# Optimization experiments

Measured on AMD Instinct MI355X. Metric: run time of the kernel, lower is better.

## Reference

```python
import jax, jax.numpy as jnp
import numpy as np
from jax import lax

B, C, H, W = 8, 64, 256, 256
K = 10  # num_experts


def conv1x1(x, w):
    # x: [B,C,H,W], w: [O,C] (1x1 conv, no bias)
    return jnp.einsum('oc,bchw->bohw', w, x)


def dyn_conv_se(x, attn, Wk, bk, gamma):
    # Dynamic_conv2d_se with with_se=True, kernel 3, stride 1, pad 1, groups=1.
    # attn: [B,K]; Wk: [K,O,I,3,3]; bk: [K,O]; gamma: [B,O]
    aw = jnp.einsum('bk,koihw->boihw', attn, Wk)        # per-sample kernels
    ab = attn @ bk                                      # [B,O]

    def one(xi, wi):
        # xi: [C,H,W], wi: [O,I,3,3]
        return lax.conv_general_dilated(
            xi[None], wi, window_strides=(1, 1), padding='SAME',
            dimension_numbers=('NCHW', 'OIHW', 'NCHW'))[0]

    y = jax.vmap(one)(x, aw) + ab[:, :, None, None]
    return y * gamma[:, :, None, None]  # SE gain


def setup_inputs() -> dict:
    key = jax.random.key(0)
    ks = jax.random.split(key, 12)
    x = jax.random.normal(ks[0], (B, C, H, W), dtype=jnp.float32)
    logits = jax.random.uniform(ks[1], (B, K), dtype=jnp.float32)
    weights = jax.nn.softmax(logits, axis=-1)
    gamma = jax.random.uniform(ks[2], (B, C), dtype=jnp.float32)
    par = jax.random.uniform(ks[3], (B, 3, 1, H, W), dtype=jnp.float32)
    s = 0.1  # default_init_weights scale
    w1 = jax.random.normal(ks[4], (K, C, C, 3, 3), dtype=jnp.float32) * s
    b1 = jax.random.normal(ks[5], (K, C), dtype=jnp.float32) * 0.01
    w2 = jax.random.normal(ks[6], (K, C, C, 3, 3), dtype=jnp.float32) * s
    b2 = jax.random.normal(ks[7], (K, C), dtype=jnp.float32) * 0.01
    w_16x16 = jax.random.normal(ks[8], (C, C), dtype=jnp.float32) * s
    w_16x8 = jax.random.normal(ks[9], (C, C), dtype=jnp.float32) * s
    w_8x8 = jax.random.normal(ks[10], (C, C), dtype=jnp.float32) * s
    return {'x': x, 'weights': weights, 'gamma': gamma, 'par': par,
            'w1': w1, 'b1': b1, 'w2': w2, 'b2': b2,
            'w_16x16': w_16x16, 'w_16x8': w_16x8, 'w_8x8': w_8x8}


def reference(x, weights, gamma, par, w1, b1, w2, b2, w_16x16, w_16x8, w_8x8):
    # channel_first=True, sparse_val=False, one_layer=False, res_scale=1
    identity = x
    dyres = (conv1x1(x, w_16x16) * par[:, 0]
             + conv1x1(x, w_16x8) * par[:, 1]
             + conv1x1(x, w_8x8) * par[:, 2])
    out = jax.nn.relu(dyn_conv_se(x, weights, w2, b2, gamma) + dyres)
    out = dyn_conv_se(out, weights, w1, b1, gamma)
    return identity + out  # res_scale = 1
```

## Files before the change

### kernel.cpp

```cpp
#include <hip/hip_runtime.h>
#include <hip/hip_bf16.h>

typedef __attribute__((ext_vector_type(8))) short short8;
typedef __attribute__((ext_vector_type(4))) float f32x4;

#define B_ 8
#define C_ 64
#define H_ 256
#define W_ 256
#define HW_ 65536
#define K_ 10
#define NS1 24
#define NS2 18
#define HP_ 258
#define WP_ 258
#define PXP_ (HP_*WP_)
#define SLABW 34
#define SLABR 6

#define NB_COMBINE 2692
#define NB_BORDER  514
#define NB_PREP    8192

static __device__ __forceinline__ unsigned short f2bf(float f) {
    __hip_bfloat16 hb = __float2bfloat16(f);
    return *(unsigned short*)&hb;
}
static __device__ __forceinline__ float bf2f(unsigned short u) {
    unsigned v = ((unsigned)u) << 16;
    float f;
    __builtin_memcpy(&f, &v, 4);
    return f;
}

static __device__ __forceinline__ void gload_lds16(const void* g, void* l) {
    __builtin_amdgcn_global_load_lds(
        (const __attribute__((address_space(1))) unsigned int*)(unsigned long long)g,
        (__attribute__((address_space(3))) unsigned int*)(unsigned int)(unsigned long long)l,
        16, 0, 0);
}

__device__ __host__ constexpr int SDW(int ii) {
    return (ii / 6 == 0) ? 0 : ((ii / 6 == 1) ? 2 : 1);
}
__device__ __host__ constexpr int SDH(int ii) { return (ii % 6) / 2; }
__device__ __host__ constexpr int SH(int ii)  { return ii & 1; }
__device__ __host__ constexpr int SS(int ii)  {
    return ii < 18 ? (3 * SDH(ii) + SDW(ii)) * 2 + SH(ii) : ii;
}

__global__ __launch_bounds__(256) void k_pre(
    const float* __restrict__ x,
    const float* __restrict__ attn, const float* __restrict__ gamma,
    const float* __restrict__ w1, const float* __restrict__ b1,
    const float* __restrict__ w2, const float* __restrict__ b2,
    const float* __restrict__ w16, const float* __restrict__ w168,
    const float* __restrict__ w88,
    unsigned short* __restrict__ W4_1, unsigned short* __restrict__ W4_2,
    float* __restrict__ bias1, float* __restrict__ bias2,
    unsigned short* __restrict__ X1p, unsigned short* __restrict__ Tp)
{
    __shared__ float ls[64][65];
    const int bx = blockIdx.x;
    const int t = threadIdx.x;

    if (bx < NB_COMBINE) {
        const int N1 = B_ * NS1 * 2048;
        const int N2 = B_ * NS2 * 2048;
        int gid = bx * 256 + t;
        if (gid < N1) {
            int b = gid / (NS1 * 2048);
            int r = gid - b * (NS1 * 2048);
            int s = r >> 11;
            int r2 = r & 2047;
            int of = r2 >> 9, l = (r2 >> 3) & 63, j = r2 & 7;
            int o = of * 16 + (l & 15);
            int g = l >> 4;
            float val;
            if (s < 18) {
                int tp = s >> 1, h = s & 1;
                int c = h * 32 + g * 8 + j;
                float acc = 0.f;
                #pragma unroll
                for (int k = 0; k < K_; ++k)
                    acc += attn[b * K_ + k] * w2[((size_t)(k * 64 + o) * 64 + c) * 9 + tp];
                val = acc * gamma[b * 64 + o];
            } else {
                int e = s - 18;
                int m = e >> 1, h = e & 1;
                int c = h * 32 + g * 8 + j;
                const float* wm = (m == 0) ? w16 : (m == 1 ? w168 : w88);
                val = wm[o * 64 + c];
            }
            W4_1[gid] = f2bf(val);
        } else if (gid < N1 + N2) {
            int gid2 = gid - N1;
            int b = gid2 / (NS2 * 2048);
            int r = gid2 - b * (NS2 * 2048);
            int s = r >> 11;
            int r2 = r & 2047;
            int of = r2 >> 9, l = (r2 >> 3) & 63, j = r2 & 7;
            int o = of * 16 + (l & 15);
            int g = l >> 4;
            int tp = s >> 1, h = s & 1;
            int c = h * 32 + g * 8 + j;
            float acc = 0.f;
            #pragma unroll
            for (int k = 0; k < K_; ++k)
                acc += attn[b * K_ + k] * w1[((size_t)(k * 64 + o) * 64 + c) * 9 + tp];
            W4_2[gid2] = f2bf(acc * gamma[b * 64 + o]);
        } else if (gid < N1 + N2 + 1024) {
            int id2 = gid - N1 - N2;
            int b = id2 >> 7;
            int rest = id2 & 127;
            int o = rest >> 1;
            int which = rest & 1;
            const float* bb = which ? b1 : b2;
            float acc = 0.f;
            #pragma unroll
            for (int k = 0; k < K_; ++k) acc += attn[b * K_ + k] * bb[k * 64 + o];
            float v = acc * gamma[b * 64 + o];
            if (which) bias2[b * 64 + o] = v; else bias1[b * 64 + o] = v;
        }
    } else if (bx < NB_COMBINE + NB_BORDER) {
        int gid = (bx - NB_COMBINE) * 256 + t;
        if (gid >= 2 * B_ * 1028 * 8) return;
        int chunk = gid & 7;
        int rest = gid >> 3;
        int p = rest % 1028;
        int rb = rest / 1028;
        int buf = rb & 1, b = rb >> 1;
        int row, col;
        if (p < 258) { row = 0; col = p; }
        else if (p < 516) { row = 257; col = p - 258; }
        else if (p < 772) { row = p - 516 + 1; col = 0; }
        else { row = p - 772 + 1; col = 257; }
        unsigned short* base = (buf ? Tp : X1p) +
            ((size_t)b * PXP_ + (size_t)row * WP_ + col) * 64 + chunk * 8;
        *(short8*)base = (short8){0, 0, 0, 0, 0, 0, 0, 0};
    } else {
        int pb = bx - (NB_COMBINE + NB_BORDER);
        const int b = pb >> 10;
        const int px0 = (pb & 1023) * 64;
        const int row = px0 >> 8;
        const int col0 = px0 & 255;
        #pragma unroll
        for (int it = 0; it < 4; ++it) {
            int e = t + it * 256;
            int ch = e >> 4, q = e & 15;
            f32x4 v = *(const f32x4*)(x + ((size_t)(b * 64 + ch)) * HW_ + px0 + q * 4);
            ls[ch][q * 4 + 0] = v[0];
            ls[ch][q * 4 + 1] = v[1];
            ls[ch][q * 4 + 2] = v[2];
            ls[ch][q * 4 + 3] = v[3];
        }
        __syncthreads();
        unsigned short* dst = X1p + ((size_t)b * PXP_ + (size_t)(row + 1) * WP_ + col0 + 1) * 64;
        #pragma unroll
        for (int k = 0; k < 2; ++k) {
            int c = t + k * 256;
            int px = c >> 3, ch0 = (c & 7) * 8;
            short8 v8;
            #pragma unroll
            for (int j = 0; j < 8; ++j) v8[j] = (short)f2bf(ls[ch0 + j][px]);
            *(short8*)(dst + (size_t)px * 64 + ch0) = v8;
        }
    }
}

template<int STAGE>
__global__ __launch_bounds__(128, 2) void k_conv(
    const unsigned short* __restrict__ Xp,
    const unsigned short* __restrict__ Xres,
    const float* __restrict__ par,
    const unsigned short* __restrict__ W4,
    const float* __restrict__ bias,
    unsigned short* __restrict__ Tp,
    float* __restrict__ Fout)
{
    constexpr int NS = (STAGE == 1) ? NS1 : NS2;
    __shared__ short xs[SLABR * SLABW * 64];
    __shared__ short bring[3 * 2048];

    const int tid = threadIdx.x;
    const int l = tid & 63;
    const int wv = tid >> 6;
    const int b = blockIdx.y;
    const int bswz = (blockIdx.x & 7) * 64 + (blockIdx.x >> 3);
    const int rblk = bswz >> 3;
    const int cblk = bswz & 7;
    const int gh0 = rblk * 4, w0 = cblk * 32;
    const int ln15 = l & 15, g = l >> 4;

    const char* XbP = (const char*)Xp + (size_t)b * PXP_ * 128;
    const unsigned short* Wb = W4 + (size_t)b * (NS * 2048);

    float pvv[3][4];
    if constexpr (STAGE == 1) {
        #pragma unroll
        for (int m = 0; m < 3; ++m)
            #pragma unroll
            for (int mf = 0; mf < 4; ++mf)
                pvv[m][mf] = par[((size_t)b * 3 + m) * HW_ +
                                 (gh0 + 2 * wv + (mf >> 1)) * W_ + w0 + 16 * (mf & 1) + ln15];
    }

    f32x4 acc[4][4];
    #pragma unroll
    for (int mf = 0; mf < 4; ++mf)
        #pragma unroll
        for (int of = 0; of < 4; ++of)
            acc[mf][of] = (f32x4){0.f, 0.f, 0.f, 0.f};

    #pragma unroll
    for (int it = 0; it < 13; ++it) {
        int tau = tid + it * 128;
        if (tau < SLABR * SLABW * 8) {
            int slot = tau & 7;
            int rest = tau >> 3;
            int px = rest % SLABW;
            int row = rest / SLABW;
            int cb = slot ^ (px & 7);
            gload_lds16(XbP + ((size_t)(gh0 + row) * WP_ + (w0 + px)) * 128 + cb * 16,
                        (char*)xs + (size_t)tau * 16);
        }
    }
    auto stage_b = [&](int ii) {
        const char* src = (const char*)Wb + (size_t)SS(ii) * 4096;
        char* dst = (char*)bring + (ii % 3) * 4096;
        gload_lds16(src + tid * 16, dst + tid * 16);
        gload_lds16(src + 2048 + tid * 16, dst + 2048 + tid * 16);
    };
    stage_b(0);
    stage_b(1);

    auto ldA = [&](int ro, int ph, int hh, int dw) -> short8 {
        int idx = 16 * ph + ln15 + dw;
        int rowx = 2 * wv + ro;
        return *(const short8*)((const char*)xs + (rowx * SLABW + idx) * 128 +
                                ((((hh << 2) | g) ^ (idx & 7)) << 4));
    };

    asm volatile("s_waitcnt vmcnt(2)" ::: "memory");
    __builtin_amdgcn_s_barrier();

    short8 ca[4][2][2];

    #pragma unroll
    for (int ii = 0; ii < 18; ++ii) {
        const int dw = SDW(ii), dh = SDH(ii), hh = SH(ii);
        if (ii + 2 < NS) stage_b(ii + 2);
        const char* rb = (const char*)bring + (ii % 3) * 4096 + (size_t)l * 16;
        short8 bf0 = *(const short8*)(rb);
        short8 bf1 = *(const short8*)(rb + 1024);
        short8 bf2 = *(const short8*)(rb + 2048);
        short8 bf3 = *(const short8*)(rb + 3072);
        if (dh == 0) {
            ca[0][0][hh] = ldA(0, 0, hh, dw);
            ca[0][1][hh] = ldA(0, 1, hh, dw);
            ca[1][0][hh] = ldA(1, 0, hh, dw);
            ca[1][1][hh] = ldA(1, 1, hh, dw);
        } else {
            ca[dh + 1][0][hh] = ldA(dh + 1, 0, hh, dw);
            ca[dh + 1][1][hh] = ldA(dh + 1, 1, hh, dw);
        }
        __builtin_amdgcn_s_setprio(1);
        #pragma unroll
        for (int mf = 0; mf < 4; ++mf) {
            short8 a = ca[(mf >> 1) + dh][mf & 1][hh];
            acc[mf][0] = __builtin_amdgcn_mfma_f32_16x16x32_bf16(a, bf0, acc[mf][0], 0, 0, 0);
            acc[mf][1] = __builtin_amdgcn_mfma_f32_16x16x32_bf16(a, bf1, acc[mf][1], 0, 0, 0);
            acc[mf][2] = __builtin_amdgcn_mfma_f32_16x16x32_bf16(a, bf2, acc[mf][2], 0, 0, 0);
            acc[mf][3] = __builtin_amdgcn_mfma_f32_16x16x32_bf16(a, bf3, acc[mf][3], 0, 0, 0);
        }
        __builtin_amdgcn_s_setprio(0);
        if (ii + 1 < NS) {
            if (ii + 2 < NS) asm volatile("s_waitcnt vmcnt(2)" ::: "memory");
            else             asm volatile("s_waitcnt vmcnt(0)" ::: "memory");
            __builtin_amdgcn_s_barrier();
        }
    }

    if constexpr (STAGE == 1) {
        #pragma unroll
        for (int ii = 18; ii < 24; ++ii) {
            const int e = ii - 18, m = e >> 1, hh = e & 1;
            if (ii + 2 < NS1) stage_b(ii + 2);
            const char* rb = (const char*)bring + (ii % 3) * 4096 + (size_t)l * 16;
            short8 bf0 = *(const short8*)(rb);
            short8 bf1 = *(const short8*)(rb + 1024);
            short8 bf2 = *(const short8*)(rb + 2048);
            short8 bf3 = *(const short8*)(rb + 3072);
            short8 sa[4];
            #pragma unroll
            for (int mf = 0; mf < 4; ++mf) {
                short8 base = ca[(mf >> 1) + 1][mf & 1][hh];
                #pragma unroll
                for (int j = 0; j < 8; ++j)
                    sa[mf][j] = (short)f2bf(bf2f((unsigned short)base[j]) * pvv[m][mf]);
            }
            __builtin_amdgcn_s_setprio(1);
            #pragma unroll
            for (int mf = 0; mf < 4; ++mf) {
                acc[mf][0] = __builtin_amdgcn_mfma_f32_16x16x32_bf16(sa[mf], bf0, acc[mf][0], 0, 0, 0);
                acc[mf][1] = __builtin_amdgcn_mfma_f32_16x16x32_bf16(sa[mf], bf1, acc[mf][1], 0, 0, 0);
                acc[mf][2] = __builtin_amdgcn_mfma_f32_16x16x32_bf16(sa[mf], bf2, acc[mf][2], 0, 0, 0);
                acc[mf][3] = __builtin_amdgcn_mfma_f32_16x16x32_bf16(sa[mf], bf3, acc[mf][3], 0, 0, 0);
            }
            __builtin_amdgcn_s_setprio(0);
            if (ii + 1 < NS1) {
                if (ii + 2 < NS1) asm volatile("s_waitcnt vmcnt(2)" ::: "memory");
                else              asm volatile("s_waitcnt vmcnt(0)" ::: "memory");
                __builtin_amdgcn_s_barrier();
            }
        }

        __syncthreads();
        unsigned short* tl = (unsigned short*)xs;
        #pragma unroll
        for (int of = 0; of < 4; ++of) {
            int o = of * 16 + ln15;
            float bi = bias[b * 64 + o];
            #pragma unroll
            for (int mf = 0; mf < 4; ++mf) {
                int row_local = 2 * wv + (mf >> 1);
                #pragma unroll
                for (int q = 0; q < 4; ++q) {
                    int px = 16 * (mf & 1) + 4 * g + q;
                    float v = fmaxf(acc[mf][of][q] + bi, 0.f);
                    tl[row_local * 2048 + px * 64 + (o ^ ((px & 7) << 3))] = f2bf(v);
                }
            }
        }
        __syncthreads();
        #pragma unroll
        for (int it = 0; it < 8; ++it) {
            int tau = tid + it * 128;
            int row = tau >> 8;
            int px = (tau >> 3) & 31;
            int j = tau & 7;
            short8 v = *(const short8*)(tl + row * 2048 + px * 64 + ((j ^ (px & 7)) * 8));
            *(short8*)(Tp + ((size_t)b * PXP_ + (size_t)(gh0 + row + 1) * WP_ +
                             (w0 + 1 + px)) * 64 + j * 8) = v;
        }
    } else {
        const unsigned short* Xr = Xres + (size_t)b * PXP_ * 64;
        #pragma unroll
        for (int of = 0; of < 4; ++of) {
            int o = of * 16 + ln15;
            float bi = bias[b * 64 + o];
            #pragma unroll
            for (int mf = 0; mf < 4; ++mf) {
                int gh = gh0 + 2 * wv + (mf >> 1);
                int gw = w0 + 16 * (mf & 1) + g * 4;
                size_t idx = ((size_t)b * 64 + o) * HW_ + (size_t)gh * W_ + gw;
                const unsigned short* xr =
                    Xr + ((size_t)(gh + 1) * WP_ + (gw + 1)) * 64 + o;
                f32x4 ov;
                #pragma unroll
                for (int q = 0; q < 4; ++q)
                    ov[q] = bf2f(xr[(size_t)q * 64]) + acc[mf][of][q] + bi;
                *(f32x4*)(Fout + idx) = ov;
            }
        }
    }
}

extern "C" void kernel_launch(void* const* d_in, const int* in_sizes, int n_in,
                              void* d_out, int out_size, void* d_ws, size_t ws_size,
                              hipStream_t stream) {
    const float* x     = (const float*)d_in[0];
    const float* attn  = (const float*)d_in[1];
    const float* gamma = (const float*)d_in[2];
    const float* par   = (const float*)d_in[3];
    const float* w1    = (const float*)d_in[4];
    const float* b1    = (const float*)d_in[5];
    const float* w2    = (const float*)d_in[6];
    const float* b2    = (const float*)d_in[7];
    const float* w16   = (const float*)d_in[8];
    const float* w168  = (const float*)d_in[9];
    const float* w88   = (const float*)d_in[10];
    float* out = (float*)d_out;

    char* w = (char*)d_ws;
    unsigned short* W4_1 = (unsigned short*)w;
    unsigned short* W4_2 = (unsigned short*)(w + 786432);
    float* bias1 = (float*)(w + 786432 + 589824);
    float* bias2 = (float*)(w + 786432 + 589824 + 2048);
    unsigned short* X1p = (unsigned short*)(w + 1380352);
    unsigned short* Tp  = (unsigned short*)(w + 1380352 + 68161536);

    k_pre<<<dim3(NB_COMBINE + NB_BORDER + NB_PREP), dim3(256), 0, stream>>>(
        x, attn, gamma, w1, b1, w2, b2, w16, w168, w88,
        W4_1, W4_2, bias1, bias2, X1p, Tp);

    dim3 grid(512, 8);
    k_conv<1><<<grid, dim3(128), 0, stream>>>(X1p, nullptr, par, W4_1, bias1, Tp, nullptr);
    k_conv<2><<<grid, dim3(128), 0, stream>>>(Tp, X1p, par, W4_2, bias2, nullptr, out);
}
```

Measured before the change: 172.5 us.

## Make conv blocks persistent over four column tiles with prefetched next slab

Each block now processes four consecutive 32-column tiles in a loop instead of one, and the grid shrinks from 512 to 128 blocks per batch. The next tile's input slab, par values and first weight stages are issued before the current tile's epilogue, so loads overlap the output writes. The stage-1 epilogue now goes through a small LDS staging area in the weight ring, one row at a time, so it does not clobber the prefetched slab. This adds many extra barriers and serialises the epilogue. The smaller grid (1024 blocks of 2 waves) may also leave CUs underused.

After: 336.2 us. 1.95x slower.

```diff
diff --git a/kernel.cpp b/kernel.cpp
--- a/kernel.cpp
+++ b/kernel.cpp
@@ -186,54 +186,45 @@
     const int l = tid & 63;
     const int wv = tid >> 6;
     const int b = blockIdx.y;
-    const int bswz = (blockIdx.x & 7) * 64 + (blockIdx.x >> 3);
-    const int rblk = bswz >> 3;
-    const int cblk = bswz & 7;
-    const int gh0 = rblk * 4, w0 = cblk * 32;
+    const int bswz = (blockIdx.x & 7) * 16 + (blockIdx.x >> 3);
+    const int rblk = bswz >> 1;
+    const int cpair = bswz & 1;
+    const int gh0 = rblk * 4;
     const int ln15 = l & 15, g = l >> 4;
 
     const char* XbP = (const char*)Xp + (size_t)b * PXP_ * 128;
     const unsigned short* Wb = W4 + (size_t)b * (NS * 2048);
 
     float pvv[3][4];
-    if constexpr (STAGE == 1) {
+    auto issue_par = [&](int w0n) {
         #pragma unroll
         for (int m = 0; m < 3; ++m)
             #pragma unroll
             for (int mf = 0; mf < 4; ++mf)
                 pvv[m][mf] = par[((size_t)b * 3 + m) * HW_ +
-                                 (gh0 + 2 * wv + (mf >> 1)) * W_ + w0 + 16 * (mf & 1) + ln15];
-    }
-
-    f32x4 acc[4][4];
-    #pragma unroll
-    for (int mf = 0; mf < 4; ++mf)
-        #pragma unroll
-        for (int of = 0; of < 4; ++of)
-            acc[mf][of] = (f32x4){0.f, 0.f, 0.f, 0.f};
-
-    #pragma unroll
-    for (int it = 0; it < 13; ++it) {
-        int tau = tid + it * 128;
-        if (tau < SLABR * SLABW * 8) {
-            int slot = tau & 7;
-            int rest = tau >> 3;
-            int px = rest % SLABW;
-            int row = rest / SLABW;
-            int cb = slot ^ (px & 7);
-            gload_lds16(XbP + ((size_t)(gh0 + row) * WP_ + (w0 + px)) * 128 + cb * 16,
-                        (char*)xs + (size_t)tau * 16);
-        }
-    }
+                                 (gh0 + 2 * wv + (mf >> 1)) * W_ + w0n + 16 * (mf & 1) + ln15];
+    };
+    auto issue_slab = [&](int w0n) {
+        #pragma unroll
+        for (int it = 0; it < 13; ++it) {
+            int tau = tid + it * 128;
+            if (tau < SLABR * SLABW * 8) {
+                int slot = tau & 7;
+                int rest = tau >> 3;
+                int px = rest % SLABW;
+                int row = rest / SLABW;
+                int cb = slot ^ (px & 7);
+                gload_lds16(XbP + ((size_t)(gh0 + row) * WP_ + (w0n + px)) * 128 + cb * 16,
+                            (char*)xs + (size_t)tau * 16);
+            }
+        }
+    };
     auto stage_b = [&](int ii) {
         const char* src = (const char*)Wb + (size_t)SS(ii) * 4096;
         char* dst = (char*)bring + (ii % 3) * 4096;
         gload_lds16(src + tid * 16, dst + tid * 16);
         gload_lds16(src + 2048 + tid * 16, dst + 2048 + tid * 16);
     };
-    stage_b(0);
-    stage_b(1);
-
     auto ldA = [&](int ro, int ph, int hh, int dw) -> short8 {
         int idx = 16 * ph + ln15 + dw;
         int rowx = 2 * wv + ro;
@@ -241,126 +232,165 @@
                                 ((((hh << 2) | g) ^ (idx & 7)) << 4));
     };
 
-    asm volatile("s_waitcnt vmcnt(2)" ::: "memory");
-    __builtin_amdgcn_s_barrier();
-
-    short8 ca[4][2][2];
-
-    #pragma unroll
-    for (int ii = 0; ii < 18; ++ii) {
-        const int dw = SDW(ii), dh = SDH(ii), hh = SH(ii);
-        if (ii + 2 < NS) stage_b(ii + 2);
-        const char* rb = (const char*)bring + (ii % 3) * 4096 + (size_t)l * 16;
-        short8 bf0 = *(const short8*)(rb);
-        short8 bf1 = *(const short8*)(rb + 1024);
-        short8 bf2 = *(const short8*)(rb + 2048);
-        short8 bf3 = *(const short8*)(rb + 3072);
-        if (dh == 0) {
-            ca[0][0][hh] = ldA(0, 0, hh, dw);
-            ca[0][1][hh] = ldA(0, 1, hh, dw);
-            ca[1][0][hh] = ldA(1, 0, hh, dw);
-            ca[1][1][hh] = ldA(1, 1, hh, dw);
-        } else {
-            ca[dh + 1][0][hh] = ldA(dh + 1, 0, hh, dw);
-            ca[dh + 1][1][hh] = ldA(dh + 1, 1, hh, dw);
-        }
-        __builtin_amdgcn_s_setprio(1);
-        #pragma unroll
-        for (int mf = 0; mf < 4; ++mf) {
-            short8 a = ca[(mf >> 1) + dh][mf & 1][hh];
-            acc[mf][0] = __builtin_amdgcn_mfma_f32_16x16x32_bf16(a, bf0, acc[mf][0], 0, 0, 0);
-            acc[mf][1] = __builtin_amdgcn_mfma_f32_16x16x32_bf16(a, bf1, acc[mf][1], 0, 0, 0);
-            acc[mf][2] = __builtin_amdgcn_mfma_f32_16x16x32_bf16(a, bf2, acc[mf][2], 0, 0, 0);
-            acc[mf][3] = __builtin_amdgcn_mfma_f32_16x16x32_bf16(a, bf3, acc[mf][3], 0, 0, 0);
-        }
-        __builtin_amdgcn_s_setprio(0);
-        if (ii + 1 < NS) {
-            if (ii + 2 < NS) asm volatile("s_waitcnt vmcnt(2)" ::: "memory");
-            else             asm volatile("s_waitcnt vmcnt(0)" ::: "memory");
-            __builtin_amdgcn_s_barrier();
-        }
+    {
+        const int w00 = cpair * 128;
+        if constexpr (STAGE == 1) issue_par(w00);
+        issue_slab(w00);
+        stage_b(0);
+        stage_b(1);
     }
 
-    if constexpr (STAGE == 1) {
-        #pragma unroll
-        for (int ii = 18; ii < 24; ++ii) {
-            const int e = ii - 18, m = e >> 1, hh = e & 1;
-            if (ii + 2 < NS1) stage_b(ii + 2);
+    #pragma unroll 1
+    for (int t = 0; t < 4; ++t) {
+        const int w0cur = cpair * 128 + t * 32;
+
+        asm volatile("s_waitcnt vmcnt(2)" ::: "memory");
+        __builtin_amdgcn_s_barrier();
+
+        f32x4 acc[4][4];
+        #pragma unroll
+        for (int mf = 0; mf < 4; ++mf)
+            #pragma unroll
+            for (int of = 0; of < 4; ++of)
+                acc[mf][of] = (f32x4){0.f, 0.f, 0.f, 0.f};
+
+        short8 ca[4][2][2];
+
+        #pragma unroll
+        for (int ii = 0; ii < 18; ++ii) {
+            const int dw = SDW(ii), dh = SDH(ii), hh = SH(ii);
+            if (ii + 2 < NS) stage_b(ii + 2);
             const char* rb = (const char*)bring + (ii % 3) * 4096 + (size_t)l * 16;
             short8 bf0 = *(const short8*)(rb);
             short8 bf1 = *(const short8*)(rb + 1024);
             short8 bf2 = *(const short8*)(rb + 2048);
             short8 bf3 = *(const short8*)(rb + 3072);
-            short8 sa[4];
+            if (dh == 0) {
+                ca[0][0][hh] = ldA(0, 0, hh, dw);
+                ca[0][1][hh] = ldA(0, 1, hh, dw);
+                ca[1][0][hh] = ldA(1, 0, hh, dw);
+                ca[1][1][hh] = ldA(1, 1, hh, dw);
+            } else {
+                ca[dh + 1][0][hh] = ldA(dh + 1, 0, hh, dw);
+                ca[dh + 1][1][hh] = ldA(dh + 1, 1, hh, dw);
+            }
+            __builtin_amdgcn_s_setprio(1);
             #pragma unroll
             for (int mf = 0; mf < 4; ++mf) {
-                short8 base = ca[(mf >> 1) + 1][mf & 1][hh];
+                short8 a = ca[(mf >> 1) + dh][mf & 1][hh];
+                acc[mf][0] = __builtin_amdgcn_mfma_f32_16x16x32_bf16(a, bf0, acc[mf][0], 0, 0, 0);
+                acc[mf][1] = __builtin_amdgcn_mfma_f32_16x16x32_bf16(a, bf1, acc[mf][1], 0, 0, 0);
+                acc[mf][2] = __builtin_amdgcn_mfma_f32_16x16x32_bf16(a, bf2, acc[mf][2], 0, 0, 0);
+                acc[mf][3] = __builtin_amdgcn_mfma_f32_16x16x32_bf16(a, bf3, acc[mf][3], 0, 0, 0);
+            }
+            __builtin_amdgcn_s_setprio(0);
+            if (ii + 1 < NS) {
+                if (ii + 2 < NS) asm volatile("s_waitcnt vmcnt(2)" ::: "memory");
+                else             asm volatile("s_waitcnt vmcnt(0)" ::: "memory");
+                __builtin_amdgcn_s_barrier();
+            }
+        }
+
+        if constexpr (STAGE == 1) {
+            #pragma unroll
+            for (int ii = 18; ii < 24; ++ii) {
+                const int e = ii - 18, m = e >> 1, hh = e & 1;
+                if (ii + 2 < NS1) stage_b(ii + 2);
+                const char* rb = (const char*)bring + (ii % 3) * 4096 + (size_t)l * 16;
+                short8 bf0 = *(const short8*)(rb);
+                short8 bf1 = *(const short8*)(rb + 1024);
+                short8 bf2 = *(const short8*)(rb + 2048);
+                short8 bf3 = *(const short8*)(rb + 3072);
+                short8 sa[4];
                 #pragma unroll
-                for (int j = 0; j < 8; ++j)
-                    sa[mf][j] = (short)f2bf(bf2f((unsigned short)base[j]) * pvv[m][mf]);
-            }
-            __builtin_amdgcn_s_setprio(1);
-            #pragma unroll
-            for (int mf = 0; mf < 4; ++mf) {
-                acc[mf][0] = __builtin_amdgcn_mfma_f32_16x16x32_bf16(sa[mf], bf0, acc[mf][0], 0, 0, 0);
-                acc[mf][1] = __builtin_amdgcn_mfma_f32_16x16x32_bf16(sa[mf], bf1, acc[mf][1], 0, 0, 0);
-                acc[mf][2] = __builtin_amdgcn_mfma_f32_16x16x32_bf16(sa[mf], bf2, acc[mf][2], 0, 0, 0);
-                acc[mf][3] = __builtin_amdgcn_mfma_f32_16x16x32_bf16(sa[mf], bf3, acc[mf][3], 0, 0, 0);
-            }
-            __builtin_amdgcn_s_setprio(0);
-            if (ii + 1 < NS1) {
-                if (ii + 2 < NS1) asm volatile("s_waitcnt vmcnt(2)" ::: "memory");
-                else              asm volatile("s_waitcnt vmcnt(0)" ::: "memory");
+                for (int mf = 0; mf < 4; ++mf) {
+                    short8 base = ca[(mf >> 1) + 1][mf & 1][hh];
+                    #pragma unroll
+                    for (int j = 0; j < 8; ++j)
+                        sa[mf][j] = (short)f2bf(bf2f((unsigned short)base[j]) * pvv[m][mf]);
+                }
+                __builtin_amdgcn_s_setprio(1);
+                #pragma unroll
+                for (int mf = 0; mf < 4; ++mf) {
+                    acc[mf][0] = __builtin_amdgcn_mfma_f32_16x16x32_bf16(sa[mf], bf0, acc[mf][0], 0, 0, 0);
+                    acc[mf][1] = __builtin_amdgcn_mfma_f32_16x16x32_bf16(sa[mf], bf1, acc[mf][1], 0, 0, 0);
+                    acc[mf][2] = __builtin_amdgcn_mfma_f32_16x16x32_bf16(sa[mf], bf2, acc[mf][2], 0, 0, 0);
+                    acc[mf][3] = __builtin_amdgcn_mfma_f32_16x16x32_bf16(sa[mf], bf3, acc[mf][3], 0, 0, 0);
+                }
+                __builtin_amdgcn_s_setprio(0);
+                if (ii + 1 < NS1) {
+                    if (ii + 2 < NS1) asm volatile("s_waitcnt vmcnt(2)" ::: "memory");
+                    else              asm volatile("s_waitcnt vmcnt(0)" ::: "memory");
+                    __builtin_amdgcn_s_barrier();
+                }
+            }
+        }
+
+        asm volatile("s_waitcnt lgkmcnt(0)" ::: "memory");
+        __builtin_amdgcn_s_barrier();
+
+        if (t < 3) {
+            const int w0n = w0cur + 32;
+            if constexpr (STAGE == 1) issue_par(w0n);
+            issue_slab(w0n);
+            stage_b(0);
+            stage_b(1);
+        }
+
+        if constexpr (STAGE == 1) {
+            unsigned short* tl4 = (unsigned short*)bring + 2 * 2048;
+            #pragma unroll
+            for (int r = 0; r < 4; ++r) {
+                if (wv == (r >> 1)) {
+                    #pragma unroll
+                    for (int of = 0; of < 4; ++of) {
+                        int o = of * 16 + ln15;
+                        float bi = bias[b * 64 + o];
+                        #pragma unroll
+                        for (int mm = 0; mm < 2; ++mm) {
+                            int mf = 2 * (r & 1) + mm;
+                            #pragma unroll
+                            for (int q = 0; q < 4; ++q) {
+                                int px = 16 * (mf & 1) + 4 * g + q;
+                                float v = fmaxf(acc[mf][of][q] + bi, 0.f);
+                                tl4[px * 64 + (o ^ ((px & 7) << 3))] = f2bf(v);
+                            }
+                        }
+                    }
+                }
+                asm volatile("s_waitcnt lgkmcnt(0)" ::: "memory");
                 __builtin_amdgcn_s_barrier();
-            }
-        }
-
-        __syncthreads();
-        unsigned short* tl = (unsigned short*)xs;
-        #pragma unroll
-        for (int of = 0; of < 4; ++of) {
-            int o = of * 16 + ln15;
-            float bi = bias[b * 64 + o];
-            #pragma unroll
-            for (int mf = 0; mf < 4; ++mf) {
-                int row_local = 2 * wv + (mf >> 1);
                 #pragma unroll
-                for (int q = 0; q < 4; ++q) {
-                    int px = 16 * (mf & 1) + 4 * g + q;
-                    float v = fmaxf(acc[mf][of][q] + bi, 0.f);
-                    tl[row_local * 2048 + px * 64 + (o ^ ((px & 7) << 3))] = f2bf(v);
-                }
-            }
-        }
-        __syncthreads();
-        #pragma unroll
-        for (int it = 0; it < 8; ++it) {
-            int tau = tid + it * 128;
-            int row = tau >> 8;
-            int px = (tau >> 3) & 31;
-            int j = tau & 7;
-            short8 v = *(const short8*)(tl + row * 2048 + px * 64 + ((j ^ (px & 7)) * 8));
-            *(short8*)(Tp + ((size_t)b * PXP_ + (size_t)(gh0 + row + 1) * WP_ +
-                             (w0 + 1 + px)) * 64 + j * 8) = v;
-        }
-    } else {
-        const unsigned short* Xr = Xres + (size_t)b * PXP_ * 64;
-        #pragma unroll
-        for (int of = 0; of < 4; ++of) {
-            int o = of * 16 + ln15;
-            float bi = bias[b * 64 + o];
-            #pragma unroll
-            for (int mf = 0; mf < 4; ++mf) {
-                int gh = gh0 + 2 * wv + (mf >> 1);
-                int gw = w0 + 16 * (mf & 1) + g * 4;
-                size_t idx = ((size_t)b * 64 + o) * HW_ + (size_t)gh * W_ + gw;
-                const unsigned short* xr =
-                    Xr + ((size_t)(gh + 1) * WP_ + (gw + 1)) * 64 + o;
-                f32x4 ov;
+                for (int it = 0; it < 2; ++it) {
+                    int tau = tid + it * 128;
+                    int px = tau >> 3;
+                    int j = tau & 7;
+                    short8 v = *(const short8*)(tl4 + px * 64 + ((j ^ (px & 7)) * 8));
+                    *(short8*)(Tp + ((size_t)b * PXP_ + (size_t)(gh0 + r + 1) * WP_ +
+                                     (w0cur + 1 + px)) * 64 + j * 8) = v;
+                }
+                asm volatile("s_waitcnt lgkmcnt(0)" ::: "memory");
+                __builtin_amdgcn_s_barrier();
+            }
+        } else {
+            const unsigned short* Xr = Xres + (size_t)b * PXP_ * 64;
+            #pragma unroll
+            for (int of = 0; of < 4; ++of) {
+                int o = of * 16 + ln15;
+                float bi = bias[b * 64 + o];
                 #pragma unroll
-                for (int q = 0; q < 4; ++q)
-                    ov[q] = bf2f(xr[(size_t)q * 64]) + acc[mf][of][q] + bi;
-                *(f32x4*)(Fout + idx) = ov;
+                for (int mf = 0; mf < 4; ++mf) {
+                    int gh = gh0 + 2 * wv + (mf >> 1);
+                    int gw = w0cur + 16 * (mf & 1) + g * 4;
+                    size_t idx = ((size_t)b * 64 + o) * HW_ + (size_t)gh * W_ + gw;
+                    const unsigned short* xr =
+                        Xr + ((size_t)(gh + 1) * WP_ + (gw + 1)) * 64 + o;
+                    f32x4 ov;
+                    #pragma unroll
+                    for (int q = 0; q < 4; ++q)
+                        ov[q] = bf2f(xr[(size_t)q * 64]) + acc[mf][of][q] + bi;
+                    *(f32x4*)(Fout + idx) = ov;
+                }
             }
         }
     }
@@ -394,7 +424,7 @@
         x, attn, gamma, w1, b1, w2, b2, w16, w168, w88,
         W4_1, W4_2, bias1, bias2, X1p, Tp);
 
-    dim3 grid(512, 8);
+    dim3 grid(128, 8);
     k_conv<1><<<grid, dim3(128), 0, stream>>>(X1p, nullptr, par, W4_1, bias1, Tp, nullptr);
     k_conv<2><<<grid, dim3(128), 0, stream>>>(Tp, X1p, par, W4_2, bias2, nullptr, out);
 }
```

## Split conv input slab into two channel halves processed sequentially to shrink LDS

Applied to the files above, without the earlier changes.

The 3x3 conv kernel now stages the input slab one 32-channel half at a time instead of all 64 channels. It runs the full 9-tap (plus 3 dyres) weight pipeline per half, with a new swizzle for the half-width slab layout. This roughly halves the slab's LDS footprint and halves the cached A-fragment registers, aiming for more resident blocks and less register pressure. In exchange the second slab load happens behind a full barrier with no overlap, and the B-ring pipeline is restarted per half.

Result: no change. 175.7 us (+1.9%).

```diff
diff --git a/kernel.cpp b/kernel.cpp
--- a/kernel.cpp
+++ b/kernel.cpp
@@ -17,6 +17,9 @@
 #define PXP_ (HP_*WP_)
 #define SLABW 34
 #define SLABR 6
+#define HSLAB_B (SLABR*SLABW*64)
+#define RING_OFF HSLAB_B
+#define LDS_TOT (HSLAB_B + 3*4096)
 
 #define NB_COMBINE 2692
 #define NB_BORDER  514
@@ -40,13 +43,12 @@
         16, 0, 0);
 }
 
-__device__ __host__ constexpr int SDW(int ii) {
-    return (ii / 6 == 0) ? 0 : ((ii / 6 == 1) ? 2 : 1);
-}
-__device__ __host__ constexpr int SDH(int ii) { return (ii % 6) / 2; }
-__device__ __host__ constexpr int SH(int ii)  { return ii & 1; }
-__device__ __host__ constexpr int SS(int ii)  {
-    return ii < 18 ? (3 * SDH(ii) + SDW(ii)) * 2 + SH(ii) : ii;
+__device__ __host__ constexpr int PDW(int jj) {
+    return (jj / 3 == 0) ? 0 : ((jj / 3 == 1) ? 2 : 1);
+}
+__device__ __host__ constexpr int PDH(int jj) { return jj % 3; }
+__device__ __host__ constexpr int PS(int h, int jj) {
+    return jj < 9 ? (PDH(jj) * 3 + PDW(jj)) * 2 + h : 18 + 2 * (jj - 9) + h;
 }
 
 __global__ __launch_bounds__(256) void k_pre(
@@ -178,9 +180,10 @@
     unsigned short* __restrict__ Tp,
     float* __restrict__ Fout)
 {
-    constexpr int NS = (STAGE == 1) ? NS1 : NS2;
-    __shared__ short xs[SLABR * SLABW * 64];
-    __shared__ short bring[3 * 2048];
+    constexpr int NP = (STAGE == 1) ? 12 : 9;
+    __shared__ char smem[LDS_TOT];
+    short* xs = (short*)smem;
+    char* bring = smem + RING_OFF;
 
     const int tid = threadIdx.x;
     const int l = tid & 63;
@@ -193,7 +196,7 @@
     const int ln15 = l & 15, g = l >> 4;
 
     const char* XbP = (const char*)Xp + (size_t)b * PXP_ * 128;
-    const unsigned short* Wb = W4 + (size_t)b * (NS * 2048);
+    const unsigned short* Wb = W4 + (size_t)b * (((STAGE == 1) ? NS1 : NS2) * 2048);
 
     float pvv[3][4];
     if constexpr (STAGE == 1) {
@@ -212,111 +215,101 @@
         for (int of = 0; of < 4; ++of)
             acc[mf][of] = (f32x4){0.f, 0.f, 0.f, 0.f};
 
-    #pragma unroll
-    for (int it = 0; it < 13; ++it) {
-        int tau = tid + it * 128;
-        if (tau < SLABR * SLABW * 8) {
-            int slot = tau & 7;
-            int rest = tau >> 3;
-            int px = rest % SLABW;
-            int row = rest / SLABW;
-            int cb = slot ^ (px & 7);
-            gload_lds16(XbP + ((size_t)(gh0 + row) * WP_ + (w0 + px)) * 128 + cb * 16,
-                        (char*)xs + (size_t)tau * 16);
-        }
-    }
-    auto stage_b = [&](int ii) {
-        const char* src = (const char*)Wb + (size_t)SS(ii) * 4096;
-        char* dst = (char*)bring + (ii % 3) * 4096;
+    auto stage_slab = [&](int h) {
+        #pragma unroll
+        for (int it = 0; it < 7; ++it) {
+            int tau = tid + it * 128;
+            if (tau < SLABR * SLABW * 4) {
+                int cs = tau & 3;
+                int rest = tau >> 2;
+                int px = rest % SLABW;
+                int row = rest / SLABW;
+                int c = cs ^ ((px >> 1) & 3);
+                gload_lds16(XbP + ((size_t)(gh0 + row) * WP_ + (w0 + px)) * 128 +
+                            (h * 4 + c) * 16,
+                            (char*)xs + (size_t)tau * 16);
+            }
+        }
+    };
+    auto stage_b = [&](int h, int jj) {
+        const char* src = (const char*)Wb + (size_t)PS(h, jj) * 4096;
+        char* dst = bring + (jj % 3) * 4096;
         gload_lds16(src + tid * 16, dst + tid * 16);
         gload_lds16(src + 2048 + tid * 16, dst + 2048 + tid * 16);
     };
-    stage_b(0);
-    stage_b(1);
-
-    auto ldA = [&](int ro, int ph, int hh, int dw) -> short8 {
+    auto ldA = [&](int ro, int ph, int dw) -> short8 {
         int idx = 16 * ph + ln15 + dw;
         int rowx = 2 * wv + ro;
-        return *(const short8*)((const char*)xs + (rowx * SLABW + idx) * 128 +
-                                ((((hh << 2) | g) ^ (idx & 7)) << 4));
+        return *(const short8*)((const char*)xs +
+                ((rowx * SLABW + idx) * 4 + (g ^ ((idx >> 1) & 3))) * 16);
     };
 
-    asm volatile("s_waitcnt vmcnt(2)" ::: "memory");
-    __builtin_amdgcn_s_barrier();
-
-    short8 ca[4][2][2];
-
     #pragma unroll
-    for (int ii = 0; ii < 18; ++ii) {
-        const int dw = SDW(ii), dh = SDH(ii), hh = SH(ii);
-        if (ii + 2 < NS) stage_b(ii + 2);
-        const char* rb = (const char*)bring + (ii % 3) * 4096 + (size_t)l * 16;
-        short8 bf0 = *(const short8*)(rb);
-        short8 bf1 = *(const short8*)(rb + 1024);
-        short8 bf2 = *(const short8*)(rb + 2048);
-        short8 bf3 = *(const short8*)(rb + 3072);
-        if (dh == 0) {
-            ca[0][0][hh] = ldA(0, 0, hh, dw);
-            ca[0][1][hh] = ldA(0, 1, hh, dw);
-            ca[1][0][hh] = ldA(1, 0, hh, dw);
-            ca[1][1][hh] = ldA(1, 1, hh, dw);
-        } else {
-            ca[dh + 1][0][hh] = ldA(dh + 1, 0, hh, dw);
-            ca[dh + 1][1][hh] = ldA(dh + 1, 1, hh, dw);
-        }
-        __builtin_amdgcn_s_setprio(1);
-        #pragma unroll
-        for (int mf = 0; mf < 4; ++mf) {
-            short8 a = ca[(mf >> 1) + dh][mf & 1][hh];
-            acc[mf][0] = __builtin_amdgcn_mfma_f32_16x16x32_bf16(a, bf0, acc[mf][0], 0, 0, 0);
-            acc[mf][1] = __builtin_amdgcn_mfma_f32_16x16x32_bf16(a, bf1, acc[mf][1], 0, 0, 0);
-            acc[mf][2] = __builtin_amdgcn_mfma_f32_16x16x32_bf16(a, bf2, acc[mf][2], 0, 0, 0);
-            acc[mf][3] = __builtin_amdgcn_mfma_f32_16x16x32_bf16(a, bf3, acc[mf][3], 0, 0, 0);
-        }
-        __builtin_amdgcn_s_setprio(0);
-        if (ii + 1 < NS) {
-            if (ii + 2 < NS) asm volatile("s_waitcnt vmcnt(2)" ::: "memory");
-            else             asm volatile("s_waitcnt vmcnt(0)" ::: "memory");
-            __builtin_amdgcn_s_barrier();
-        }
-    }
-
-    if constexpr (STAGE == 1) {
-        #pragma unroll
-        for (int ii = 18; ii < 24; ++ii) {
-            const int e = ii - 18, m = e >> 1, hh = e & 1;
-            if (ii + 2 < NS1) stage_b(ii + 2);
-            const char* rb = (const char*)bring + (ii % 3) * 4096 + (size_t)l * 16;
+    for (int h = 0; h < 2; ++h) {
+        stage_slab(h);
+        stage_b(h, 0);
+        stage_b(h, 1);
+        asm volatile("s_waitcnt vmcnt(2)" ::: "memory");
+        __builtin_amdgcn_s_barrier();
+
+        short8 ca[4][2];
+
+        #pragma unroll
+        for (int jj = 0; jj < NP; ++jj) {
+            if (jj + 2 < NP) stage_b(h, jj + 2);
+            const char* rb = bring + (jj % 3) * 4096 + (size_t)l * 16;
             short8 bf0 = *(const short8*)(rb);
             short8 bf1 = *(const short8*)(rb + 1024);
             short8 bf2 = *(const short8*)(rb + 2048);
             short8 bf3 = *(const short8*)(rb + 3072);
-            short8 sa[4];
+
+            short8 a[4];
+            if (jj < 9) {
+                const int dw = PDW(jj), dh = PDH(jj);
+                if (dh == 0) {
+                    ca[0][0] = ldA(0, 0, dw);
+                    ca[0][1] = ldA(0, 1, dw);
+                    ca[1][0] = ldA(1, 0, dw);
+                    ca[1][1] = ldA(1, 1, dw);
+                } else {
+                    ca[dh + 1][0] = ldA(dh + 1, 0, dw);
+                    ca[dh + 1][1] = ldA(dh + 1, 1, dw);
+                }
+                #pragma unroll
+                for (int mf = 0; mf < 4; ++mf) a[mf] = ca[(mf >> 1) + dh][mf & 1];
+            } else {
+                const int m = jj - 9;
+                #pragma unroll
+                for (int mf = 0; mf < 4; ++mf) {
+                    short8 base = ca[(mf >> 1) + 1][mf & 1];
+                    #pragma unroll
+                    for (int j = 0; j < 8; ++j)
+                        a[mf][j] = (short)f2bf(bf2f((unsigned short)base[j]) * pvv[m][mf]);
+                }
+            }
+
+            __builtin_amdgcn_s_setprio(1);
             #pragma unroll
             for (int mf = 0; mf < 4; ++mf) {
-                short8 base = ca[(mf >> 1) + 1][mf & 1][hh];
-                #pragma unroll
-                for (int j = 0; j < 8; ++j)
-                    sa[mf][j] = (short)f2bf(bf2f((unsigned short)base[j]) * pvv[m][mf]);
-            }
-            __builtin_amdgcn_s_setprio(1);
-            #pragma unroll
-            for (int mf = 0; mf < 4; ++mf) {
-                acc[mf][0] = __builtin_amdgcn_mfma_f32_16x16x32_bf16(sa[mf], bf0, acc[mf][0], 0, 0, 0);
-                acc[mf][1] = __builtin_amdgcn_mfma_f32_16x16x32_bf16(sa[mf], bf1, acc[mf][1], 0, 0, 0);
-                acc[mf][2] = __builtin_amdgcn_mfma_f32_16x16x32_bf16(sa[mf], bf2, acc[mf][2], 0, 0, 0);
-                acc[mf][3] = __builtin_amdgcn_mfma_f32_16x16x32_bf16(sa[mf], bf3, acc[mf][3], 0, 0, 0);
+                acc[mf][0] = __builtin_amdgcn_mfma_f32_16x16x32_bf16(a[mf], bf0, acc[mf][0], 0, 0, 0);
+                acc[mf][1] = __builtin_amdgcn_mfma_f32_16x16x32_bf16(a[mf], bf1, acc[mf][1], 0, 0, 0);
+                acc[mf][2] = __builtin_amdgcn_mfma_f32_16x16x32_bf16(a[mf], bf2, acc[mf][2], 0, 0, 0);
+                acc[mf][3] = __builtin_amdgcn_mfma_f32_16x16x32_bf16(a[mf], bf3, acc[mf][3], 0, 0, 0);
             }
             __builtin_amdgcn_s_setprio(0);
-            if (ii + 1 < NS1) {
-                if (ii + 2 < NS1) asm volatile("s_waitcnt vmcnt(2)" ::: "memory");
-                else              asm volatile("s_waitcnt vmcnt(0)" ::: "memory");
+
+            if (jj + 1 < NP) {
+                if (jj + 2 < NP) asm volatile("s_waitcnt vmcnt(2)" ::: "memory");
+                else             asm volatile("s_waitcnt vmcnt(0)" ::: "memory");
                 __builtin_amdgcn_s_barrier();
             }
         }
-
-        __syncthreads();
-        unsigned short* tl = (unsigned short*)xs;
+        asm volatile("s_waitcnt vmcnt(0) lgkmcnt(0)" ::: "memory");
+        __builtin_amdgcn_s_barrier();
+    }
+
+    if constexpr (STAGE == 1) {
+        unsigned short* tl = (unsigned short*)smem;
         #pragma unroll
         for (int of = 0; of < 4; ++of) {
             int o = of * 16 + ln15;
```
